# Kernel tuning notes

Measured on AMD Instinct MI355X. Metric: run time of the kernel, lower is better.

The kernel has to match this reference:

```python
import jax, jax.numpy as jnp
import numpy as np

B, H, W, C = 32, 224, 224, 3
HID = 64


def setup_inputs() -> dict:
    key = jax.random.key(0)
    k0, k1, k2 = jax.random.split(key, 3)
    inputs = jax.random.normal(k0, (B, H, W, C), dtype=jnp.float32)
    # Localization-net dense params. Original uses zeros init (identity transform);
    # we use small random weights plus the identity affine bias so the sampling
    # grid is a nontrivial perturbation of identity.
    w1 = jax.random.normal(k1, (H * W * C, HID), dtype=jnp.float32) * 1e-3
    b1 = jnp.zeros((HID,), dtype=jnp.float32)
    w2 = jax.random.normal(k2, (HID, 6), dtype=jnp.float32) * 1e-2
    b2 = jnp.array([1.0, 0.0, 0.0, 0.0, 1.0, 0.0], dtype=jnp.float32)
    return {"inputs": inputs, "w1": w1, "b1": b1, "w2": w2, "b2": b2}


def _bilinear_sampler(img, x_s, y_s):
    # img: [B,H,W,C]; x_s, y_s: [B,H,W] normalized coords in [-1,1]
    Bn, Hn, Wn, Cn = img.shape
    x = 0.5 * (x_s + 1.0) * (Wn - 1)
    y = 0.5 * (y_s + 1.0) * (Hn - 1)
    x0 = jnp.floor(x).astype(jnp.int32)
    x1 = x0 + 1
    y0 = jnp.floor(y).astype(jnp.int32)
    y1 = y0 + 1
    x0c = jnp.clip(x0, 0, Wn - 1)
    x1c = jnp.clip(x1, 0, Wn - 1)
    y0c = jnp.clip(y0, 0, Hn - 1)
    y1c = jnp.clip(y1, 0, Hn - 1)
    b_idx = jnp.arange(Bn, dtype=jnp.int32)[:, None, None]
    Ia = img[b_idx, y0c, x0c]  # [B,H,W,C]
    Ib = img[b_idx, y1c, x0c]
    Ic = img[b_idx, y0c, x1c]
    Id = img[b_idx, y1c, x1c]
    x0f = x0c.astype(x.dtype)
    x1f = x1c.astype(x.dtype)
    y0f = y0c.astype(y.dtype)
    y1f = y1c.astype(y.dtype)
    wa = ((x1f - x) * (y1f - y))[..., None]
    wb = ((x1f - x) * (y - y0f))[..., None]
    wc = ((x - x0f) * (y1f - y))[..., None]
    wd = ((x - x0f) * (y - y0f))[..., None]
    return wa * Ia + wb * Ib + wc * Ic + wd * Id


def reference(inputs, w1, b1, w2, b2):
    Bn, Hn, Wn, Cn = inputs.shape
    # NOTE: original keras code overwrites the conv branch with flatten(inputs),
    # so the conv/maxpool layers are dead code and omitted. Dropout is identity
    # at inference (training=False).
    flat = inputs.reshape(Bn, -1)
    h = jnp.tanh(flat @ w1 + b1)
    theta = jnp.tanh(h @ w2 + b2).reshape(Bn, 2, 3)
    # affine sampling grid over normalized target coords
    xt, yt = jnp.meshgrid(
        jnp.linspace(-1.0, 1.0, Wn, dtype=inputs.dtype),
        jnp.linspace(-1.0, 1.0, Hn, dtype=inputs.dtype),
    )  # each [H,W]
    grid = jnp.stack([xt.ravel(), yt.ravel(), jnp.ones_like(xt).ravel()])  # [3,H*W]
    batch_grid = jnp.einsum("bij,jk->bik", theta, grid).reshape(Bn, 2, Hn, Wn)
    x_s = batch_grid[:, 0]
    y_s = batch_grid[:, 1]
    return _bilinear_sampler(inputs, x_s, y_s)
```

## Files before the change

### kernel.cpp

```cpp
#include <hip/hip_runtime.h>

#define BATCH 32
#define HDIM 224
#define WDIM 224
#define CDIM 3
#define KTOT (HDIM * WDIM * CDIM)
#define HID 64
#define KCHUNK 128
#define NBLK1 (KTOT / KCHUNK)
#define PIX (HDIM * WDIM)
#define BLK3 (PIX / 256)

__global__ __launch_bounds__(256, 5) void k1_gemm(const float* __restrict__ flat,
                                                  const float* __restrict__ w1,
                                                  float* __restrict__ hacc) {
    __shared__ float smem[8192];
    const int tid  = threadIdx.x;
    const int lane = tid & 63;
    const int wave = tid >> 6;
    const int k0   = blockIdx.x * KCHUNK;

#pragma unroll
    for (int t = 0; t < 4; ++t) {
        const int idx = tid + t * 256;
        const int b   = idx >> 5;
        const int kq  = idx & 31;
        const float4 v = *(const float4*)(flat + (size_t)b * KTOT + k0 + kq * 4);
        *(float4*)(smem + b * 128 + kq * 4) = v;
    }
    __syncthreads();

    float acc[32];
#pragma unroll
    for (int j = 0; j < 32; ++j) acc[j] = 0.0f;

    const int kw = wave * 32;
#pragma unroll
    for (int kk = 0; kk < 32; kk += 4) {
        const int k = k0 + kw + kk;
        float w[4];
#pragma unroll
        for (int i = 0; i < 4; ++i)
            w[i] = w1[(size_t)(k + i) * HID + lane];
#pragma unroll
        for (int bg = 0; bg < 4; ++bg) {
            float4 x[8];
#pragma unroll
            for (int j = 0; j < 8; ++j)
                x[j] = *(const float4*)(smem + (bg * 8 + j) * 128 + kw + kk);
#pragma unroll
            for (int i = 0; i < 4; ++i)
#pragma unroll
                for (int j = 0; j < 8; ++j)
                    acc[bg * 8 + j] = fmaf(((const float*)&x[j])[i], w[i],
                                           acc[bg * 8 + j]);
        }
    }
    __syncthreads();

#pragma unroll
    for (int j = 0; j < 32; ++j)
        smem[wave * 2048 + j * 64 + lane] = acc[j];
    __syncthreads();

#pragma unroll
    for (int t = 0; t < 8; ++t) {
        const int idx = tid + t * 256;
        const float s = smem[idx] + smem[2048 + idx] +
                        smem[4096 + idx] + smem[6144 + idx];
        atomicAdd(hacc + idx, s);
    }
}

__global__ __launch_bounds__(256) void k2_head(const float* __restrict__ hacc,
                                               const float* __restrict__ b1,
                                               const float* __restrict__ w2,
                                               const float* __restrict__ b2,
                                               float* __restrict__ theta) {
    __shared__ float h[BATCH * HID];
    const int tid = threadIdx.x;
    for (int idx = tid; idx < BATCH * HID; idx += 256)
        h[idx] = tanhf(hacc[idx] + b1[idx & (HID - 1)]);
    __syncthreads();
    if (tid < BATCH * 6) {
        const int b = tid / 6;
        const int j = tid - b * 6;
        float s = b2[j];
#pragma unroll
        for (int t = 0; t < HID; ++t)
            s = fmaf(h[b * HID + t], w2[t * 6 + j], s);
        theta[tid] = tanhf(s);
    }
}

__global__ __launch_bounds__(256) void k3_sample(const float* __restrict__ img,
                                                 const float* __restrict__ theta,
                                                 float* __restrict__ out) {
    const int b   = blockIdx.x / BLK3;
    const int pix = (blockIdx.x - b * BLK3) * 256 + threadIdx.x;
    const int i   = pix / WDIM;
    const int j   = pix - i * WDIM;

    const float* th = theta + b * 6;
    const float t0 = th[0], t1 = th[1], t2 = th[2];
    const float t3 = th[3], t4 = th[4], t5 = th[5];

    const float xt = (2.0f * (float)j - (float)(WDIM - 1)) / (float)(WDIM - 1);
    const float yt = (2.0f * (float)i - (float)(HDIM - 1)) / (float)(HDIM - 1);

    const float xs = t0 * xt + t1 * yt + t2;
    const float ys = t3 * xt + t4 * yt + t5;

    const float x = 0.5f * (xs + 1.0f) * (float)(WDIM - 1);
    const float y = 0.5f * (ys + 1.0f) * (float)(HDIM - 1);

    const int x0 = (int)floorf(x);
    const int y0 = (int)floorf(y);
    const int x1 = x0 + 1;
    const int y1 = y0 + 1;

    const int x0c = min(max(x0, 0), WDIM - 1);
    const int x1c = min(max(x1, 0), WDIM - 1);
    const int y0c = min(max(y0, 0), HDIM - 1);
    const int y1c = min(max(y1, 0), HDIM - 1);

    const float x0f = (float)x0c, x1f = (float)x1c;
    const float y0f = (float)y0c, y1f = (float)y1c;

    const float wa = (x1f - x) * (y1f - y);
    const float wb = (x1f - x) * (y - y0f);
    const float wc = (x - x0f) * (y1f - y);
    const float wd = (x - x0f) * (y - y0f);

    const float* base = img + (size_t)b * KTOT;
    const float* pa = base + (size_t)(y0c * WDIM + x0c) * 3;
    const float* pb = base + (size_t)(y1c * WDIM + x0c) * 3;
    const float* pc = base + (size_t)(y0c * WDIM + x1c) * 3;
    const float* pd = base + (size_t)(y1c * WDIM + x1c) * 3;

    float* po = out + (size_t)b * KTOT + (size_t)pix * 3;
#pragma unroll
    for (int c = 0; c < 3; ++c)
        po[c] = wa * pa[c] + wb * pb[c] + wc * pc[c] + wd * pd[c];
}

extern "C" void kernel_launch(void* const* d_in, const int* in_sizes, int n_in,
                              void* d_out, int out_size, void* d_ws, size_t ws_size,
                              hipStream_t stream) {
    const float* inputs = (const float*)d_in[0];
    const float* w1     = (const float*)d_in[1];
    const float* b1     = (const float*)d_in[2];
    const float* w2     = (const float*)d_in[3];
    const float* b2     = (const float*)d_in[4];
    float* out = (float*)d_out;

    float* hacc  = (float*)d_ws;
    float* theta = hacc + BATCH * HID;

    hipMemsetAsync(hacc, 0, BATCH * HID * sizeof(float), stream);
    k1_gemm<<<NBLK1, 256, 0, stream>>>(inputs, w1, hacc);
    k2_head<<<1, 256, 0, stream>>>(hacc, b1, w2, b2, theta);
    k3_sample<<<BATCH * BLK3, 256, 0, stream>>>(inputs, theta, out);
}
```

Before: 142.0 us.

## Fuse head into sampler, preload w1 in registers, vectorize sampler stores

Removes the separate single-block head kernel by having every sampler block recompute tanh(hidden) and theta for its batch, saving one launch at the cost of redundant tiny work per block. The GEMM kernel now loads all 32 w1 values per thread up front, uses a simpler per-batch loop, and reduces partials through 3/4 of the shared memory, with wave 0 doing the atomics. The sampler processes 4 pixels per thread and writes three float4 stores instead of scalar stores.

```diff
diff --git a/kernel.cpp b/kernel.cpp
--- a/kernel.cpp
+++ b/kernel.cpp
@@ -9,24 +9,31 @@
 #define KCHUNK 128
 #define NBLK1 (KTOT / KCHUNK)
 #define PIX (HDIM * WDIM)
-#define BLK3 (PIX / 256)
+#define BLK3 49
 
 __global__ __launch_bounds__(256, 5) void k1_gemm(const float* __restrict__ flat,
                                                   const float* __restrict__ w1,
                                                   float* __restrict__ hacc) {
-    __shared__ float smem[8192];
+    __shared__ float smem[6144];
     const int tid  = threadIdx.x;
     const int lane = tid & 63;
     const int wave = tid >> 6;
     const int k0   = blockIdx.x * KCHUNK;
+    const int kw   = wave * 32;
+
+    float w[32];
+    const float* wp = w1 + (size_t)(k0 + kw) * HID + lane;
+#pragma unroll
+    for (int i = 0; i < 32; ++i)
+        w[i] = wp[(size_t)i * HID];
 
 #pragma unroll
     for (int t = 0; t < 4; ++t) {
         const int idx = tid + t * 256;
         const int b   = idx >> 5;
         const int kq  = idx & 31;
-        const float4 v = *(const float4*)(flat + (size_t)b * KTOT + k0 + kq * 4);
-        *(float4*)(smem + b * 128 + kq * 4) = v;
+        *(float4*)(smem + idx * 4) =
+            *(const float4*)(flat + (size_t)b * KTOT + k0 + kq * 4);
     }
     __syncthreads();
 
@@ -34,114 +41,113 @@
 #pragma unroll
     for (int j = 0; j < 32; ++j) acc[j] = 0.0f;
 
-    const int kw = wave * 32;
 #pragma unroll
     for (int kk = 0; kk < 32; kk += 4) {
-        const int k = k0 + kw + kk;
-        float w[4];
 #pragma unroll
-        for (int i = 0; i < 4; ++i)
-            w[i] = w1[(size_t)(k + i) * HID + lane];
-#pragma unroll
-        for (int bg = 0; bg < 4; ++bg) {
-            float4 x[8];
-#pragma unroll
-            for (int j = 0; j < 8; ++j)
-                x[j] = *(const float4*)(smem + (bg * 8 + j) * 128 + kw + kk);
-#pragma unroll
-            for (int i = 0; i < 4; ++i)
-#pragma unroll
-                for (int j = 0; j < 8; ++j)
-                    acc[bg * 8 + j] = fmaf(((const float*)&x[j])[i], w[i],
-                                           acc[bg * 8 + j]);
+        for (int b = 0; b < 32; ++b) {
+            const float4 x = *(const float4*)(smem + b * 128 + kw + kk);
+            float a = acc[b];
+            a = fmaf(x.x, w[kk + 0], a);
+            a = fmaf(x.y, w[kk + 1], a);
+            a = fmaf(x.z, w[kk + 2], a);
+            a = fmaf(x.w, w[kk + 3], a);
+            acc[b] = a;
         }
     }
     __syncthreads();
 
+    if (wave) {
 #pragma unroll
-    for (int j = 0; j < 32; ++j)
-        smem[wave * 2048 + j * 64 + lane] = acc[j];
+        for (int j = 0; j < 32; ++j)
+            smem[(wave - 1) * 2048 + j * 64 + lane] = acc[j];
+    }
     __syncthreads();
-
+    if (wave == 0) {
 #pragma unroll
-    for (int t = 0; t < 8; ++t) {
-        const int idx = tid + t * 256;
-        const float s = smem[idx] + smem[2048 + idx] +
-                        smem[4096 + idx] + smem[6144 + idx];
-        atomicAdd(hacc + idx, s);
-    }
-}
-
-__global__ __launch_bounds__(256) void k2_head(const float* __restrict__ hacc,
-                                               const float* __restrict__ b1,
-                                               const float* __restrict__ w2,
-                                               const float* __restrict__ b2,
-                                               float* __restrict__ theta) {
-    __shared__ float h[BATCH * HID];
-    const int tid = threadIdx.x;
-    for (int idx = tid; idx < BATCH * HID; idx += 256)
-        h[idx] = tanhf(hacc[idx] + b1[idx & (HID - 1)]);
-    __syncthreads();
-    if (tid < BATCH * 6) {
-        const int b = tid / 6;
-        const int j = tid - b * 6;
-        float s = b2[j];
-#pragma unroll
-        for (int t = 0; t < HID; ++t)
-            s = fmaf(h[b * HID + t], w2[t * 6 + j], s);
-        theta[tid] = tanhf(s);
+        for (int j = 0; j < 32; ++j) {
+            const int idx = j * 64 + lane;
+            atomicAdd(hacc + idx,
+                      acc[j] + smem[idx] + smem[2048 + idx] + smem[4096 + idx]);
+        }
     }
 }
 
 __global__ __launch_bounds__(256) void k3_sample(const float* __restrict__ img,
-                                                 const float* __restrict__ theta,
+                                                 const float* __restrict__ hacc,
+                                                 const float* __restrict__ b1,
+                                                 const float* __restrict__ w2,
+                                                 const float* __restrict__ b2,
                                                  float* __restrict__ out) {
-    const int b   = blockIdx.x / BLK3;
-    const int pix = (blockIdx.x - b * BLK3) * 256 + threadIdx.x;
-    const int i   = pix / WDIM;
-    const int j   = pix - i * WDIM;
+    const int b     = blockIdx.x / BLK3;
+    const int strip = blockIdx.x - b * BLK3;
+    const int tid   = threadIdx.x;
 
-    const float* th = theta + b * 6;
-    const float t0 = th[0], t1 = th[1], t2 = th[2];
-    const float t3 = th[3], t4 = th[4], t5 = th[5];
+    __shared__ float sh[HID];
+    __shared__ float sth[6];
+    if (tid < HID)
+        sh[tid] = tanhf(hacc[b * HID + tid] + b1[tid]);
+    __syncthreads();
+    if (tid < 6) {
+        float s = b2[tid];
+#pragma unroll
+        for (int t = 0; t < HID; ++t)
+            s = fmaf(sh[t], w2[t * 6 + tid], s);
+        sth[tid] = tanhf(s);
+    }
+    __syncthreads();
 
-    const float xt = (2.0f * (float)j - (float)(WDIM - 1)) / (float)(WDIM - 1);
-    const float yt = (2.0f * (float)i - (float)(HDIM - 1)) / (float)(HDIM - 1);
-
-    const float xs = t0 * xt + t1 * yt + t2;
-    const float ys = t3 * xt + t4 * yt + t5;
-
-    const float x = 0.5f * (xs + 1.0f) * (float)(WDIM - 1);
-    const float y = 0.5f * (ys + 1.0f) * (float)(HDIM - 1);
-
-    const int x0 = (int)floorf(x);
-    const int y0 = (int)floorf(y);
-    const int x1 = x0 + 1;
-    const int y1 = y0 + 1;
-
-    const int x0c = min(max(x0, 0), WDIM - 1);
-    const int x1c = min(max(x1, 0), WDIM - 1);
-    const int y0c = min(max(y0, 0), HDIM - 1);
-    const int y1c = min(max(y1, 0), HDIM - 1);
-
-    const float x0f = (float)x0c, x1f = (float)x1c;
-    const float y0f = (float)y0c, y1f = (float)y1c;
-
-    const float wa = (x1f - x) * (y1f - y);
-    const float wb = (x1f - x) * (y - y0f);
-    const float wc = (x - x0f) * (y1f - y);
-    const float wd = (x - x0f) * (y - y0f);
+    const float t0 = sth[0], t1 = sth[1], t2 = sth[2];
+    const float t3 = sth[3], t4 = sth[4], t5 = sth[5];
 
     const float* base = img + (size_t)b * KTOT;
-    const float* pa = base + (size_t)(y0c * WDIM + x0c) * 3;
-    const float* pb = base + (size_t)(y1c * WDIM + x0c) * 3;
-    const float* pc = base + (size_t)(y0c * WDIM + x1c) * 3;
-    const float* pd = base + (size_t)(y1c * WDIM + x1c) * 3;
+    const int pix0 = strip * 1024 + tid * 4;
 
-    float* po = out + (size_t)b * KTOT + (size_t)pix * 3;
+    float res[12];
 #pragma unroll
-    for (int c = 0; c < 3; ++c)
-        po[c] = wa * pa[c] + wb * pb[c] + wc * pc[c] + wd * pd[c];
+    for (int p = 0; p < 4; ++p) {
+        const int pix = pix0 + p;
+        const int i = pix / WDIM;
+        const int j = pix - i * WDIM;
+
+        const float xt = (2.0f * (float)j - (float)(WDIM - 1)) / (float)(WDIM - 1);
+        const float yt = (2.0f * (float)i - (float)(HDIM - 1)) / (float)(HDIM - 1);
+
+        const float xs = t0 * xt + t1 * yt + t2;
+        const float ys = t3 * xt + t4 * yt + t5;
+
+        const float x = 0.5f * (xs + 1.0f) * (float)(WDIM - 1);
+        const float y = 0.5f * (ys + 1.0f) * (float)(HDIM - 1);
+
+        const int x0 = (int)floorf(x);
+        const int y0 = (int)floorf(y);
+
+        const int x0c = min(max(x0, 0), WDIM - 1);
+        const int x1c = min(max(x0 + 1, 0), WDIM - 1);
+        const int y0c = min(max(y0, 0), HDIM - 1);
+        const int y1c = min(max(y0 + 1, 0), HDIM - 1);
+
+        const float x0f = (float)x0c, x1f = (float)x1c;
+        const float y0f = (float)y0c, y1f = (float)y1c;
+
+        const float wa = (x1f - x) * (y1f - y);
+        const float wb = (x1f - x) * (y - y0f);
+        const float wc = (x - x0f) * (y1f - y);
+        const float wd = (x - x0f) * (y - y0f);
+
+        const float* pa = base + (size_t)(y0c * WDIM + x0c) * 3;
+        const float* pb = base + (size_t)(y1c * WDIM + x0c) * 3;
+        const float* pc = base + (size_t)(y0c * WDIM + x1c) * 3;
+        const float* pd = base + (size_t)(y1c * WDIM + x1c) * 3;
+
+#pragma unroll
+        for (int c = 0; c < 3; ++c)
+            res[p * 3 + c] = wa * pa[c] + wb * pb[c] + wc * pc[c] + wd * pd[c];
+    }
+
+    float4* po = (float4*)(out + (size_t)b * KTOT + (size_t)pix0 * 3);
+    po[0] = make_float4(res[0], res[1], res[2],  res[3]);
+    po[1] = make_float4(res[4], res[5], res[6],  res[7]);
+    po[2] = make_float4(res[8], res[9], res[10], res[11]);
 }
 
 extern "C" void kernel_launch(void* const* d_in, const int* in_sizes, int n_in,
@@ -154,11 +160,9 @@
     const float* b2     = (const float*)d_in[4];
     float* out = (float*)d_out;
 
-    float* hacc  = (float*)d_ws;
-    float* theta = hacc + BATCH * HID;
+    float* hacc = (float*)d_ws;
 
     hipMemsetAsync(hacc, 0, BATCH * HID * sizeof(float), stream);
     k1_gemm<<<NBLK1, 256, 0, stream>>>(inputs, w1, hacc);
-    k2_head<<<1, 256, 0, stream>>>(hacc, b1, w2, b2, theta);
-    k3_sample<<<BATCH * BLK3, 256, 0, stream>>>(inputs, theta, out);
+    k3_sample<<<BATCH * BLK3, 256, 0, stream>>>(inputs, hacc, b1, w2, b2, out);
 }
```

Result: no change. 141.4 us (-0.4%).
